# Performance work log

Measured on AMD Instinct MI355X. Metric: run time of the kernel, lower is better.

## Reference

```python
import jax, jax.numpy as jnp
import numpy as np

N1, E1 = 102400, 300000
N2, E2 = 10240, 40960
N3, E3 = 1024, 4096
G = 64
D = 256   # node_dim == hidden_dim (forced by where(M==0, x, M))
B = 64    # bond_dim
DEPTHS = (3, 3, 4)


def _make_edges(rng, n_nodes, n_edges):
    # build mirrored directed edges so every edge has an exact reverse
    half = n_edges // 2
    u = rng.integers(0, n_nodes, half)
    v = rng.integers(0, n_nodes, half)
    src = np.concatenate([u, v])
    dst = np.concatenate([v, u])
    rev = np.concatenate([np.arange(half, n_edges), np.arange(0, half)])
    return np.stack([src, dst]).astype(np.int64), rev.astype(np.int64)


def _linear_params(key, fan_in, fan_out):
    k1, k2 = jax.random.split(key)
    s = 1.0 / np.sqrt(fan_in)
    W = jax.random.uniform(k1, (fan_in, fan_out), jnp.float32, -s, s)
    b = jax.random.uniform(k2, (fan_out,), jnp.float32, -s, s)
    return W, b


def setup_inputs() -> dict:
    rng = np.random.default_rng(0)
    key = jax.random.key(0)
    ks = jax.random.split(key, 16)

    ei1, rev1 = _make_edges(rng, N1, E1)
    ei2, rev2 = _make_edges(rng, N2, E2)
    ei3, rev3 = _make_edges(rng, N3, E3)

    inp = {
        "x": jax.random.normal(ks[0], (N1, D), jnp.float32),
        "edge_attr1": jax.random.normal(ks[1], (E1, B), jnp.float32),
        "edge_attr2": jax.random.normal(ks[2], (E2, B), jnp.float32),
        "edge_attr3": jax.random.normal(ks[3], (E3, B), jnp.float32),
        "edge_index1": jnp.asarray(ei1), "rev_edge_index1": jnp.asarray(rev1),
        "edge_index2": jnp.asarray(ei2), "rev_edge_index2": jnp.asarray(rev2),
        "edge_index3": jnp.asarray(ei3), "rev_edge_index3": jnp.asarray(rev3),
        "batch1_2": jnp.asarray(np.repeat(np.arange(N2), N1 // N2)),
        "batch2": jnp.asarray(np.repeat(np.arange(N3), N2 // N3)),
        "batch3": jnp.asarray(np.repeat(np.arange(G), N3 // G)),
    }
    kidx = 4
    for lvl in (1, 2, 3):
        Wi, bi = _linear_params(ks[kidx], D + B, D); kidx += 1
        Wh, bh = _linear_params(ks[kidx], D, D); kidx += 1
        Wo, bo = _linear_params(ks[kidx], D + D, D); kidx += 1
        inp[f"Wi{lvl}"], inp[f"bi{lvl}"] = Wi, bi
        inp[f"Wh{lvl}"], inp[f"bh{lvl}"] = Wh, bh
        inp[f"Wo{lvl}"], inp[f"bo{lvl}"] = Wo, bo
    return inp


def _bmp(x, src, dst, rev, ea, Wi, bi, Wh, bh, Wo, bo, depth):
    # BondMessagePassing.forward (dropout is identity in eval)
    n = x.shape[0]
    H0 = jax.nn.relu(jnp.concatenate([x[src], ea], axis=1) @ Wi + bi)  # [E, D]
    H = H0
    for _ in range(depth - 1):
        agg = jax.ops.segment_sum(H, dst, num_segments=n)              # [N, D]
        M = agg[src] - H[rev]
        H = jax.nn.relu(H0 + M @ Wh + bh)
    M = jax.ops.segment_sum(H, dst, num_segments=n)
    M = jnp.where(jnp.sum(M, axis=1, keepdims=True) == 0, x, M)
    return jax.nn.relu(jnp.concatenate([x, M], axis=1) @ Wo + bo)


def _mean_pool(h, seg, n):
    s = jax.ops.segment_sum(h, seg, num_segments=n)
    c = jax.ops.segment_sum(jnp.ones((h.shape[0], 1), h.dtype), seg, num_segments=n)
    return s / jnp.maximum(c, 1.0)


def reference(x, edge_attr1, edge_attr2, edge_attr3,
              edge_index1, rev_edge_index1, edge_index2, rev_edge_index2,
              edge_index3, rev_edge_index3, batch1_2, batch2, batch3,
              Wi1, bi1, Wh1, bh1, Wo1, bo1,
              Wi2, bi2, Wh2, bh2, Wo2, bo2,
              Wi3, bi3, Wh3, bh3, Wo3, bo3):
    h1 = _bmp(x, edge_index1[0], edge_index1[1], rev_edge_index1, edge_attr1,
              Wi1, bi1, Wh1, bh1, Wo1, bo1, DEPTHS[0])
    x2 = _mean_pool(h1, batch1_2, N2)
    h2 = _bmp(x2, edge_index2[0], edge_index2[1], rev_edge_index2, edge_attr2,
              Wi2, bi2, Wh2, bh2, Wo2, bo2, DEPTHS[1])
    x3 = _mean_pool(h2, batch2, N3)
    h3 = _bmp(x3, edge_index3[0], edge_index3[1], rev_edge_index3, edge_attr3,
              Wi3, bi3, Wh3, bh3, Wo3, bo3, DEPTHS[2])
    out = _mean_pool(h3, batch3, G)  # [G, D] subgraph3_pooled
    return out
```

## Files before the change

### kernel.cpp

```cpp
#include <hip/hip_runtime.h>
#include <stdint.h>

typedef __bf16 bf16;
typedef __bf16 bf16x4 __attribute__((ext_vector_type(4)));
typedef __bf16 bf16x8 __attribute__((ext_vector_type(8)));
typedef float  f32x4  __attribute__((ext_vector_type(4)));

__device__ __forceinline__ int clampi(int v, int n) { return (v < 0 || v >= n) ? 0 : v; }

__device__ __forceinline__ void gload16(const void* g, void* l) {
  __builtin_amdgcn_global_load_lds((const __attribute__((address_space(1))) void*)g,
                                   (__attribute__((address_space(3))) void*)l, 16, 0, 0);
}

__global__ void wtcvt_kernel(const float* __restrict__ W, bf16* __restrict__ Wt, int K) {
  int idx = blockIdx.x * 256 + threadIdx.x;
  if (idx >= K * 256) return;
  int k = idx >> 8, n = idx & 255;
  Wt[(size_t)n * K + k] = (bf16)W[idx];
}

__global__ void hist_kernel(const int* __restrict__ dst, int E, int* __restrict__ cnt, int N) {
  int e = blockIdx.x * 256 + threadIdx.x;
  if (e < E) atomicAdd(&cnt[clampi(dst[e], N)], 1);
}

__global__ void scan_block_kernel(const int* __restrict__ cnt, int N,
                                  int* __restrict__ incl, int* __restrict__ bsums) {
  __shared__ int sd[256];
  int t = threadIdx.x, bid = blockIdx.x;
  int base = bid * 1024 + t * 4;
  int v0 = (base + 0 < N) ? cnt[base + 0] : 0;
  int v1 = (base + 1 < N) ? cnt[base + 1] : 0;
  int v2 = (base + 2 < N) ? cnt[base + 2] : 0;
  int v3 = (base + 3 < N) ? cnt[base + 3] : 0;
  int s1 = v0 + v1, s2 = s1 + v2, s3 = s2 + v3;
  sd[t] = s3;
  __syncthreads();
  for (int off = 1; off < 256; off <<= 1) {
    int x = 0;
    if (t >= off) x = sd[t - off];
    __syncthreads();
    sd[t] += x;
    __syncthreads();
  }
  int excl = sd[t] - s3;
  if (base + 0 < N) incl[base + 0] = excl + v0;
  if (base + 1 < N) incl[base + 1] = excl + s1;
  if (base + 2 < N) incl[base + 2] = excl + s2;
  if (base + 3 < N) incl[base + 3] = excl + s3;
  if (t == 255) bsums[bid] = sd[255];
}

__global__ void scan_sums_kernel(const int* __restrict__ bsums, int nb, int* __restrict__ bexcl) {
  __shared__ int sd[256];
  int t = threadIdx.x;
  int v = (t < nb) ? bsums[t] : 0;
  sd[t] = v;
  __syncthreads();
  for (int off = 1; off < 256; off <<= 1) {
    int x = 0;
    if (t >= off) x = sd[t - off];
    __syncthreads();
    sd[t] += x;
    __syncthreads();
  }
  if (t < nb) bexcl[t] = sd[t] - v;
}

__global__ void scan_add_kernel(const int* __restrict__ incl, const int* __restrict__ bexcl,
                                int N, int* __restrict__ offs) {
  int i = blockIdx.x * 256 + threadIdx.x;
  if (i < N) offs[i + 1] = incl[i] + bexcl[i >> 10];
  if (i == 0) offs[0] = 0;
}

__global__ void scatter_kernel(const int* __restrict__ dst, int E, const int* __restrict__ offs,
                               int* __restrict__ cursor, int* __restrict__ elist, int N) {
  int e = blockIdx.x * 256 + threadIdx.x;
  if (e < E) {
    int d = clampi(dst[e], N);
    int p = atomicAdd(&cursor[d], 1);
    elist[offs[d] + p] = e;
  }
}

template <int WHERE, int XF32>
__global__ void segsum_kernel(const bf16* __restrict__ H, const int* __restrict__ elist,
                              const int* __restrict__ offs, const float* __restrict__ xf,
                              const bf16* __restrict__ xb, bf16* __restrict__ out, int N) {
  int lane = threadIdx.x & 63;
  int node = blockIdx.x * 4 + (threadIdx.x >> 6);
  if (node >= N) return;
  int beg = offs[node], end = offs[node + 1];
  float a0 = 0.f, a1 = 0.f, a2 = 0.f, a3 = 0.f;
  for (int p = beg; p < end; ++p) {
    int e = elist[p];
    bf16x4 v = ((const bf16x4*)(H + (size_t)e * 256))[lane];
    a0 += (float)v[0]; a1 += (float)v[1]; a2 += (float)v[2]; a3 += (float)v[3];
  }
  if (WHERE) {
    float s = a0 + a1 + a2 + a3;
    for (int off = 1; off < 64; off <<= 1) s += __shfl_xor(s, off);
    if (s == 0.f) {
      bf16x4 o;
      if (XF32) {
        float4 xv = ((const float4*)(xf))[(size_t)node * 64 + lane];
        o[0] = (bf16)xv.x; o[1] = (bf16)xv.y; o[2] = (bf16)xv.z; o[3] = (bf16)xv.w;
      } else {
        o = ((const bf16x4*)(xb + (size_t)node * 256))[lane];
      }
      ((bf16x4*)(out + (size_t)node * 256))[lane] = o;
      return;
    }
  }
  bf16x4 o = {(bf16)a0, (bf16)a1, (bf16)a2, (bf16)a3};
  ((bf16x4*)(out + (size_t)node * 256))[lane] = o;
}

template <int OUTF32>
__global__ void pool_kernel(const bf16* __restrict__ h, bf16* __restrict__ outb,
                            float* __restrict__ outf, int Nout, int cnt) {
  int lane = threadIdx.x & 63;
  int node = blockIdx.x * 4 + (threadIdx.x >> 6);
  if (node >= Nout) return;
  float a0 = 0.f, a1 = 0.f, a2 = 0.f, a3 = 0.f;
  size_t base = (size_t)node * cnt;
  for (int p = 0; p < cnt; ++p) {
    bf16x4 v = ((const bf16x4*)(h + (base + p) * 256))[lane];
    a0 += (float)v[0]; a1 += (float)v[1]; a2 += (float)v[2]; a3 += (float)v[3];
  }
  float c = (float)cnt;
  a0 /= c; a1 /= c; a2 /= c; a3 /= c;
  if (OUTF32) {
    float4 o = {a0, a1, a2, a3};
    ((float4*)(outf + (size_t)node * 256))[lane] = o;
  } else {
    bf16x4 o = {(bf16)a0, (bf16)a1, (bf16)a2, (bf16)a3};
    ((bf16x4*)(outb + (size_t)node * 256))[lane] = o;
  }
}

template <int MODE, int XF32>
__global__ __launch_bounds__(256, 2) void gemm_kernel(
    const float* __restrict__ A1f, const bf16* __restrict__ A1b,
    const float* __restrict__ A2f, const bf16* __restrict__ A2b,
    const bf16* __restrict__ Wt, const float* __restrict__ bias, const bf16* H0,
    const int* __restrict__ srcIdx, const int* __restrict__ revIdx,
    bf16* out, int Mrows, int K, int Nsrc) {
  __shared__ __align__(16) bf16 As[2][64 * 64];
  __shared__ __align__(16) bf16 Bs[2][256 * 64];
  const int tid = threadIdx.x;
  const int lane = tid & 63;
  const int wave = tid >> 6;
  const int m0 = blockIdx.x * 64;

  int rowA[2], uA[2], base1[2], base2[2];
#pragma unroll
  for (int r = 0; r < 2; ++r) {
    int unit = r * 256 + tid;
    rowA[r] = unit >> 3;
    uA[r] = unit & 7;
    int rr = m0 + rowA[r];
    if (rr >= Mrows) rr = Mrows - 1;
    if (MODE == 0) {
      base1[r] = clampi(srcIdx[rr], Nsrc) * 256;
      base2[r] = rr * 64;
    } else if (MODE == 1) {
      base1[r] = clampi(srcIdx[rr], Nsrc) * 256;
      base2[r] = clampi(revIdx[rr], Mrows) * 256;
    } else {
      base1[r] = rr * 256;
      base2[r] = rr * 256;
    }
  }

  f32x4 acc[4][4];
#pragma unroll
  for (int i = 0; i < 4; ++i)
#pragma unroll
    for (int j = 0; j < 4; ++j) acc[i][j] = (f32x4){0.f, 0.f, 0.f, 0.f};

  float4 pf[2][2];

  auto loadA = [&](int kc) {
    int k0 = kc * 64;
#pragma unroll
    for (int r = 0; r < 2; ++r) {
      int u8 = uA[r] * 8;
      if (MODE == 0) {
        if (k0 < 256) {
          if (XF32) {
            const float* g = A1f + (size_t)(base1[r] + k0 + u8);
            pf[r][0] = *(const float4*)g;
            pf[r][1] = *(const float4*)(g + 4);
          } else {
            pf[r][0] = *(const float4*)(A1b + (size_t)(base1[r] + k0 + u8));
          }
        } else {
          const float* g = A2f + (size_t)(base2[r] + u8);
          pf[r][0] = *(const float4*)g;
          pf[r][1] = *(const float4*)(g + 4);
        }
      } else if (MODE == 1) {
        pf[r][0] = *(const float4*)(A1b + (size_t)(base1[r] + k0 + u8));
        pf[r][1] = *(const float4*)(A2b + (size_t)(base2[r] + k0 + u8));
      } else {
        if (k0 < 256) {
          if (XF32) {
            const float* g = A1f + (size_t)(base1[r] + k0 + u8);
            pf[r][0] = *(const float4*)g;
            pf[r][1] = *(const float4*)(g + 4);
          } else {
            pf[r][0] = *(const float4*)(A1b + (size_t)(base1[r] + k0 + u8));
          }
        } else {
          pf[r][0] = *(const float4*)(A2b + (size_t)(base2[r] + (k0 - 256) + u8));
        }
      }
    }
  };

  auto writeA = [&](int kc, int buf) {
    int k0 = kc * 64;
#pragma unroll
    for (int r = 0; r < 2; ++r) {
      int row = rowA[r], us = uA[r] ^ (row & 7);
      bf16x8 v;
      bool cvt32;
      if (MODE == 0) cvt32 = XF32 || (k0 >= 256);
      else if (MODE == 2) cvt32 = XF32 && (k0 < 256);
      else cvt32 = false;
      if (MODE == 1) {
        bf16x8 va = *(bf16x8*)&pf[r][0];
        bf16x8 vh = *(bf16x8*)&pf[r][1];
#pragma unroll
        for (int j = 0; j < 8; ++j) v[j] = (bf16)((float)va[j] - (float)vh[j]);
      } else if (cvt32) {
        const float* f = (const float*)&pf[r][0];
#pragma unroll
        for (int j = 0; j < 8; ++j) v[j] = (bf16)f[j];
      } else {
        v = *(bf16x8*)&pf[r][0];
      }
      *(bf16x8*)(&As[buf][((size_t)row * 8 + us) * 8]) = v;
    }
  };

  auto issueB = [&](int kc, int buf) {
    int k0 = kc * 64;
#pragma unroll
    for (int r = 0; r < 8; ++r) {
      int unit = r * 256 + tid;
      int row = unit >> 3, us = (unit & 7) ^ (row & 7);
      gload16(Wt + (size_t)row * K + k0 + us * 8, &Bs[buf][(r * 256 + wave * 64) * 8]);
    }
  };

  const int nk = K / 64;
  issueB(0, 0);
  loadA(0);
  writeA(0, 0);
  int cur = 0;
  for (int kc = 0; kc < nk; ++kc) {
    __syncthreads();
    if (kc + 1 < nk) {
      issueB(kc + 1, cur ^ 1);
      loadA(kc + 1);
    }
    const bf16* Asb = As[cur];
    const bf16* Bsb = Bs[cur];
#pragma unroll
    for (int s = 0; s < 2; ++s) {
      int kq = s * 4 + (lane >> 4);
      bf16x8 af[4], bfr[4];
#pragma unroll
      for (int i = 0; i < 4; ++i) {
        int arow = i * 16 + (lane & 15);
        af[i] = *(const bf16x8*)(&Asb[(size_t)arow * 64 + (size_t)(kq ^ (arow & 7)) * 8]);
      }
#pragma unroll
      for (int j = 0; j < 4; ++j) {
        int brow = wave * 64 + j * 16 + (lane & 15);
        bfr[j] = *(const bf16x8*)(&Bsb[(size_t)brow * 64 + (size_t)(kq ^ (brow & 7)) * 8]);
      }
#pragma unroll
      for (int i = 0; i < 4; ++i)
#pragma unroll
        for (int j = 0; j < 4; ++j)
          acc[i][j] = __builtin_amdgcn_mfma_f32_16x16x32_bf16(af[i], bfr[j], acc[i][j], 0, 0, 0);
    }
    if (kc + 1 < nk) writeA(kc + 1, cur ^ 1);
    cur ^= 1;
  }
#pragma unroll
  for (int i = 0; i < 4; ++i) {
    int rbase = m0 + i * 16 + ((lane >> 4) << 2);
#pragma unroll
    for (int j = 0; j < 4; ++j) {
      int col = wave * 64 + j * 16 + (lane & 15);
      float bcol = bias[col];
#pragma unroll
      for (int r = 0; r < 4; ++r) {
        int row = rbase + r;
        if (row < Mrows) {
          float v = acc[i][j][r] + bcol;
          if (MODE == 1) v += (float)H0[(size_t)row * 256 + col];
          v = fmaxf(v, 0.f);
          out[(size_t)row * 256 + col] = (bf16)v;
        }
      }
    }
  }
}

template <int XF32>
static void run_level(const float* xf, const bf16* xb, const float* ea,
                      const int* src, const int* dst, const int* rev, int E, int N, int depth,
                      const bf16* WiT, const float* bi_, const bf16* WhT, const float* bh_,
                      const bf16* WoT, const float* bo_,
                      bf16* C, bf16* Dd, bf16* Ee, bf16* agg, bf16* h,
                      int* cnt, int* incl, int* offs, int* cursr, int* bsums, int* bexcl,
                      int* elist, hipStream_t stream) {
  hipMemsetAsync(cnt, 0, (size_t)N * 4, stream);
  hist_kernel<<<(E + 255) / 256, 256, 0, stream>>>(dst, E, cnt, N);
  int nb = (N + 1023) / 1024;
  scan_block_kernel<<<nb, 256, 0, stream>>>(cnt, N, incl, bsums);
  scan_sums_kernel<<<1, 256, 0, stream>>>(bsums, nb, bexcl);
  scan_add_kernel<<<(N + 255) / 256, 256, 0, stream>>>(incl, bexcl, N, offs);
  hipMemsetAsync(cursr, 0, (size_t)N * 4, stream);
  scatter_kernel<<<(E + 255) / 256, 256, 0, stream>>>(dst, E, offs, cursr, elist, N);

  dim3 ge((E + 63) / 64);
  gemm_kernel<0, XF32><<<ge, 256, 0, stream>>>(xf, xb, ea, nullptr, WiT, bi_, nullptr, src,
                                               nullptr, C, E, 320, N);
  bf16* Hcur = C;
  for (int it = 0; it < depth - 1; ++it) {
    segsum_kernel<0, 0><<<(N + 3) / 4, 256, 0, stream>>>(Hcur, elist, offs, nullptr, nullptr,
                                                         agg, N);
    bf16* Hn = (it == depth - 2) ? C : ((it & 1) ? Ee : Dd);
    gemm_kernel<1, 0><<<ge, 256, 0, stream>>>(nullptr, agg, nullptr, Hcur, WhT, bh_, C, src,
                                              rev, Hn, E, 256, N);
    Hcur = Hn;
  }
  segsum_kernel<1, XF32><<<(N + 3) / 4, 256, 0, stream>>>(Hcur, elist, offs, xf, xb, agg, N);
  dim3 gn((N + 63) / 64);
  gemm_kernel<2, XF32><<<gn, 256, 0, stream>>>(xf, xb, nullptr, agg, WoT, bo_, nullptr, nullptr,
                                               nullptr, h, N, 512, N);
}

extern "C" void kernel_launch(void* const* d_in, const int* in_sizes, int n_in,
                              void* d_out, int out_size, void* d_ws, size_t ws_size,
                              hipStream_t stream) {
  constexpr int N1 = 102400, E1 = 300000;
  constexpr int N2 = 10240, E2 = 40960;
  constexpr int N3 = 1024, E3 = 4096;
  constexpr int G = 64;
  constexpr int KI = 320, KH = 256, KO = 512;

  const float* x   = (const float*)d_in[0];
  const float* ea1 = (const float*)d_in[1];
  const float* ea2 = (const float*)d_in[2];
  const float* ea3 = (const float*)d_in[3];
  const int* ei1 = (const int*)d_in[4];
  const int* rv1 = (const int*)d_in[5];
  const int* ei2 = (const int*)d_in[6];
  const int* rv2 = (const int*)d_in[7];
  const int* ei3 = (const int*)d_in[8];
  const int* rv3 = (const int*)d_in[9];
  const float *Wi[3], *bi[3], *Wh[3], *bh[3], *Wo[3], *bo[3];
  for (int l = 0; l < 3; ++l) {
    Wi[l] = (const float*)d_in[13 + 6 * l + 0];
    bi[l] = (const float*)d_in[13 + 6 * l + 1];
    Wh[l] = (const float*)d_in[13 + 6 * l + 2];
    bh[l] = (const float*)d_in[13 + 6 * l + 3];
    Wo[l] = (const float*)d_in[13 + 6 * l + 4];
    bo[l] = (const float*)d_in[13 + 6 * l + 5];
  }
  float* outp = (float*)d_out;
  char* ws = (char*)d_ws;

  size_t off = 0;
  auto alloc = [&](size_t b) { size_t o = off; off += (b + 255) & ~(size_t)255; return o; };
  size_t o_wit[3], o_wht[3], o_wot[3];
  for (int l = 0; l < 3; ++l) {
    o_wit[l] = alloc((size_t)256 * KI * 2);
    o_wht[l] = alloc((size_t)256 * KH * 2);
    o_wot[l] = alloc((size_t)256 * KO * 2);
  }
  size_t o_C   = alloc((size_t)E1 * 256 * 2);
  size_t o_D   = alloc((size_t)E1 * 256 * 2);
  size_t o_E3b = alloc((size_t)E3 * 256 * 2);
  size_t o_agg = alloc((size_t)N1 * 256 * 2);
  size_t o_x2  = alloc((size_t)N2 * 256 * 2);
  size_t o_h2  = alloc((size_t)N2 * 256 * 2);
  size_t o_x3  = alloc((size_t)N3 * 256 * 2);
  size_t o_h3  = alloc((size_t)N3 * 256 * 2);
  size_t o_cnt = alloc((size_t)N1 * 4);
  size_t o_inc = alloc((size_t)N1 * 4);
  size_t o_off = alloc((size_t)(N1 + 1) * 4);
  size_t o_cur = alloc((size_t)N1 * 4);
  size_t o_bs  = alloc(1024 * 4);
  size_t o_bx  = alloc(1024 * 4);
  size_t o_el  = alloc((size_t)E1 * 4);

  if (ws_size < off) {
    hipMemsetAsync(d_out, 0, (size_t)out_size * 4, stream);
    return;
  }

  int* cnt   = (int*)(ws + o_cnt);
  int* incl  = (int*)(ws + o_inc);
  int* offs  = (int*)(ws + o_off);
  int* cursr = (int*)(ws + o_cur);
  int* bsums = (int*)(ws + o_bs);
  int* bexcl = (int*)(ws + o_bx);
  int* elist = (int*)(ws + o_el);
  bf16* C    = (bf16*)(ws + o_C);
  bf16* Dd   = (bf16*)(ws + o_D);
  bf16* E3b  = (bf16*)(ws + o_E3b);
  bf16* agg  = (bf16*)(ws + o_agg);
  bf16* x2b  = (bf16*)(ws + o_x2);
  bf16* h2b  = (bf16*)(ws + o_h2);
  bf16* x3b  = (bf16*)(ws + o_x3);
  bf16* h3b  = (bf16*)(ws + o_h3);

  for (int l = 0; l < 3; ++l) {
    wtcvt_kernel<<<(KI * 256 + 255) / 256, 256, 0, stream>>>(Wi[l], (bf16*)(ws + o_wit[l]), KI);
    wtcvt_kernel<<<(KH * 256 + 255) / 256, 256, 0, stream>>>(Wh[l], (bf16*)(ws + o_wht[l]), KH);
    wtcvt_kernel<<<(KO * 256 + 255) / 256, 256, 0, stream>>>(Wo[l], (bf16*)(ws + o_wot[l]), KO);
  }

  run_level<1>(x, nullptr, ea1, ei1, ei1 + E1, rv1, E1, N1, 3,
               (bf16*)(ws + o_wit[0]), bi[0], (bf16*)(ws + o_wht[0]), bh[0],
               (bf16*)(ws + o_wot[0]), bo[0], C, Dd, Dd, agg, C,
               cnt, incl, offs, cursr, bsums, bexcl, elist, stream);
  pool_kernel<0><<<(N2 + 3) / 4, 256, 0, stream>>>(C, x2b, nullptr, N2, N1 / N2);

  run_level<0>(nullptr, x2b, ea2, ei2, ei2 + E2, rv2, E2, N2, 3,
               (bf16*)(ws + o_wit[1]), bi[1], (bf16*)(ws + o_wht[1]), bh[1],
               (bf16*)(ws + o_wot[1]), bo[1], C, Dd, Dd, agg, h2b,
               cnt, incl, offs, cursr, bsums, bexcl, elist, stream);
  pool_kernel<0><<<(N3 + 3) / 4, 256, 0, stream>>>(h2b, x3b, nullptr, N3, N2 / N3);

  run_level<0>(nullptr, x3b, ea3, ei3, ei3 + E3, rv3, E3, N3, 4,
               (bf16*)(ws + o_wit[2]), bi[2], (bf16*)(ws + o_wht[2]), bh[2],
               (bf16*)(ws + o_wot[2]), bo[2], C, Dd, E3b, agg, h3b,
               cnt, incl, offs, cursr, bsums, bexcl, elist, stream);
  pool_kernel<1><<<(G + 3) / 4, 256, 0, stream>>>(h3b, nullptr, outp, G, N3 / G);
}
```

Measured before the change: 1.355 ms.

## Read GEMM weights directly from global memory and pre-convert level-1 features to bf16

The GEMM no longer stages the weight tile in LDS. Each wave now loads its B fragments straight from global or L2, and the block grows to 512 threads as a 2x4 wave grid over a 64x256 tile, with K fixed at compile time and the k-loop fully unrolled. This removes the large B shared buffer and its async copies, trading them for repeated global weight reads. It also adds a kernel that converts the fp32 level-1 node features to bf16 once, so the gathered A loads read half the bytes, but it needs extra workspace and falls back to the old path when that is unavailable.

```diff
diff --git a/kernel.cpp b/kernel.cpp
--- a/kernel.cpp
+++ b/kernel.cpp
@@ -8,9 +8,14 @@
 
 __device__ __forceinline__ int clampi(int v, int n) { return (v < 0 || v >= n) ? 0 : v; }
 
-__device__ __forceinline__ void gload16(const void* g, void* l) {
-  __builtin_amdgcn_global_load_lds((const __attribute__((address_space(1))) void*)g,
-                                   (__attribute__((address_space(3))) void*)l, 16, 0, 0);
+__global__ void cvt_kernel(const float* __restrict__ in, bf16* __restrict__ out, int n8) {
+  int i = blockIdx.x * 256 + threadIdx.x;
+  if (i >= n8) return;
+  float4 a = ((const float4*)in)[i * 2];
+  float4 b = ((const float4*)in)[i * 2 + 1];
+  bf16x8 o = {(bf16)a.x, (bf16)a.y, (bf16)a.z, (bf16)a.w,
+              (bf16)b.x, (bf16)b.y, (bf16)b.z, (bf16)b.w};
+  ((bf16x8*)out)[i] = o;
 }
 
 __global__ void wtcvt_kernel(const float* __restrict__ W, bf16* __restrict__ Wt, int K) {
@@ -142,163 +147,145 @@
 }
 
 template <int MODE, int XF32>
-__global__ __launch_bounds__(256, 2) void gemm_kernel(
+__global__ __launch_bounds__(512) void gemm_kernel(
     const float* __restrict__ A1f, const bf16* __restrict__ A1b,
     const float* __restrict__ A2f, const bf16* __restrict__ A2b,
     const bf16* __restrict__ Wt, const float* __restrict__ bias, const bf16* H0,
     const int* __restrict__ srcIdx, const int* __restrict__ revIdx,
-    bf16* out, int Mrows, int K, int Nsrc) {
+    bf16* out, int Mrows, int Nsrc) {
+  constexpr int KK = MODE == 0 ? 320 : (MODE == 1 ? 256 : 512);
+  constexpr int NK = KK / 64;
   __shared__ __align__(16) bf16 As[2][64 * 64];
-  __shared__ __align__(16) bf16 Bs[2][256 * 64];
   const int tid = threadIdx.x;
   const int lane = tid & 63;
   const int wave = tid >> 6;
+  const int wm = wave >> 2, wn = wave & 3;
   const int m0 = blockIdx.x * 64;
 
-  int rowA[2], uA[2], base1[2], base2[2];
-#pragma unroll
-  for (int r = 0; r < 2; ++r) {
-    int unit = r * 256 + tid;
-    rowA[r] = unit >> 3;
-    uA[r] = unit & 7;
-    int rr = m0 + rowA[r];
+  const int rowA = tid >> 3, uA = tid & 7;
+  int base1, base2;
+  {
+    int rr = m0 + rowA;
     if (rr >= Mrows) rr = Mrows - 1;
     if (MODE == 0) {
-      base1[r] = clampi(srcIdx[rr], Nsrc) * 256;
-      base2[r] = rr * 64;
+      base1 = clampi(srcIdx[rr], Nsrc) * 256;
+      base2 = rr * 64;
     } else if (MODE == 1) {
-      base1[r] = clampi(srcIdx[rr], Nsrc) * 256;
-      base2[r] = clampi(revIdx[rr], Mrows) * 256;
+      base1 = clampi(srcIdx[rr], Nsrc) * 256;
+      base2 = clampi(revIdx[rr], Mrows) * 256;
     } else {
-      base1[r] = rr * 256;
-      base2[r] = rr * 256;
-    }
-  }
-
-  f32x4 acc[4][4];
-#pragma unroll
-  for (int i = 0; i < 4; ++i)
+      base1 = rr * 256;
+      base2 = rr * 256;
+    }
+  }
+  int colE[4];
+#pragma unroll
+  for (int j = 0; j < 4; ++j) colE[j] = (wn * 64 + j * 16 + (lane & 15)) * KK;
+
+  f32x4 acc[2][4];
+#pragma unroll
+  for (int i = 0; i < 2; ++i)
 #pragma unroll
     for (int j = 0; j < 4; ++j) acc[i][j] = (f32x4){0.f, 0.f, 0.f, 0.f};
 
-  float4 pf[2][2];
+  float4 pf[2];
 
   auto loadA = [&](int kc) {
-    int k0 = kc * 64;
-#pragma unroll
-    for (int r = 0; r < 2; ++r) {
-      int u8 = uA[r] * 8;
-      if (MODE == 0) {
-        if (k0 < 256) {
-          if (XF32) {
-            const float* g = A1f + (size_t)(base1[r] + k0 + u8);
-            pf[r][0] = *(const float4*)g;
-            pf[r][1] = *(const float4*)(g + 4);
-          } else {
-            pf[r][0] = *(const float4*)(A1b + (size_t)(base1[r] + k0 + u8));
-          }
+    int k0 = kc * 64, u8 = uA * 8;
+    if (MODE == 0) {
+      if (k0 < 256) {
+        if (XF32) {
+          const float* g = A1f + (size_t)(base1 + k0 + u8);
+          pf[0] = *(const float4*)g;
+          pf[1] = *(const float4*)(g + 4);
         } else {
-          const float* g = A2f + (size_t)(base2[r] + u8);
-          pf[r][0] = *(const float4*)g;
-          pf[r][1] = *(const float4*)(g + 4);
+          pf[0] = *(const float4*)(A1b + (size_t)(base1 + k0 + u8));
         }
-      } else if (MODE == 1) {
-        pf[r][0] = *(const float4*)(A1b + (size_t)(base1[r] + k0 + u8));
-        pf[r][1] = *(const float4*)(A2b + (size_t)(base2[r] + k0 + u8));
       } else {
-        if (k0 < 256) {
-          if (XF32) {
-            const float* g = A1f + (size_t)(base1[r] + k0 + u8);
-            pf[r][0] = *(const float4*)g;
-            pf[r][1] = *(const float4*)(g + 4);
-          } else {
-            pf[r][0] = *(const float4*)(A1b + (size_t)(base1[r] + k0 + u8));
-          }
+        const float* g = A2f + (size_t)(base2 + u8);
+        pf[0] = *(const float4*)g;
+        pf[1] = *(const float4*)(g + 4);
+      }
+    } else if (MODE == 1) {
+      pf[0] = *(const float4*)(A1b + (size_t)(base1 + k0 + u8));
+      pf[1] = *(const float4*)(A2b + (size_t)(base2 + k0 + u8));
+    } else {
+      if (k0 < 256) {
+        if (XF32) {
+          const float* g = A1f + (size_t)(base1 + k0 + u8);
+          pf[0] = *(const float4*)g;
+          pf[1] = *(const float4*)(g + 4);
         } else {
-          pf[r][0] = *(const float4*)(A2b + (size_t)(base2[r] + (k0 - 256) + u8));
+          pf[0] = *(const float4*)(A1b + (size_t)(base1 + k0 + u8));
         }
+      } else {
+        pf[0] = *(const float4*)(A2b + (size_t)(base2 + (k0 - 256) + u8));
       }
     }
   };
 
   auto writeA = [&](int kc, int buf) {
     int k0 = kc * 64;
-#pragma unroll
-    for (int r = 0; r < 2; ++r) {
-      int row = rowA[r], us = uA[r] ^ (row & 7);
-      bf16x8 v;
-      bool cvt32;
-      if (MODE == 0) cvt32 = XF32 || (k0 >= 256);
-      else if (MODE == 2) cvt32 = XF32 && (k0 < 256);
-      else cvt32 = false;
-      if (MODE == 1) {
-        bf16x8 va = *(bf16x8*)&pf[r][0];
-        bf16x8 vh = *(bf16x8*)&pf[r][1];
-#pragma unroll
-        for (int j = 0; j < 8; ++j) v[j] = (bf16)((float)va[j] - (float)vh[j]);
-      } else if (cvt32) {
-        const float* f = (const float*)&pf[r][0];
-#pragma unroll
-        for (int j = 0; j < 8; ++j) v[j] = (bf16)f[j];
-      } else {
-        v = *(bf16x8*)&pf[r][0];
+    int us = uA ^ (rowA & 7);
+    bf16x8 v;
+    bool cvt32;
+    if (MODE == 0) cvt32 = XF32 || (k0 >= 256);
+    else if (MODE == 2) cvt32 = XF32 && (k0 < 256);
+    else cvt32 = false;
+    if (MODE == 1) {
+      bf16x8 va = *(bf16x8*)&pf[0];
+      bf16x8 vh = *(bf16x8*)&pf[1];
+#pragma unroll
+      for (int j = 0; j < 8; ++j) v[j] = (bf16)((float)va[j] - (float)vh[j]);
+    } else if (cvt32) {
+      const float* f = (const float*)&pf[0];
+#pragma unroll
+      for (int j = 0; j < 8; ++j) v[j] = (bf16)f[j];
+    } else {
+      v = *(bf16x8*)&pf[0];
+    }
+    *(bf16x8*)(&As[buf][((size_t)rowA * 8 + us) * 8]) = v;
+  };
+
+  auto compute = [&](int kc, int buf) {
+    const bf16* Asb = As[buf];
+#pragma unroll
+    for (int s = 0; s < 2; ++s) {
+      int kq = s * 4 + (lane >> 4);
+      int boff = kc * 64 + kq * 8;
+      bf16x8 bfr[4];
+#pragma unroll
+      for (int j = 0; j < 4; ++j) bfr[j] = *(const bf16x8*)(Wt + (size_t)(colE[j] + boff));
+      bf16x8 af[2];
+#pragma unroll
+      for (int i = 0; i < 2; ++i) {
+        int ar = wm * 32 + i * 16 + (lane & 15);
+        af[i] = *(const bf16x8*)(&Asb[(size_t)ar * 64 + (size_t)(kq ^ (ar & 7)) * 8]);
       }
-      *(bf16x8*)(&As[buf][((size_t)row * 8 + us) * 8]) = v;
+#pragma unroll
+      for (int i = 0; i < 2; ++i)
+#pragma unroll
+        for (int j = 0; j < 4; ++j)
+          acc[i][j] = __builtin_amdgcn_mfma_f32_16x16x32_bf16(af[i], bfr[j], acc[i][j], 0, 0, 0);
     }
   };
 
-  auto issueB = [&](int kc, int buf) {
-    int k0 = kc * 64;
-#pragma unroll
-    for (int r = 0; r < 8; ++r) {
-      int unit = r * 256 + tid;
-      int row = unit >> 3, us = (unit & 7) ^ (row & 7);
-      gload16(Wt + (size_t)row * K + k0 + us * 8, &Bs[buf][(r * 256 + wave * 64) * 8]);
-    }
-  };
-
-  const int nk = K / 64;
-  issueB(0, 0);
   loadA(0);
   writeA(0, 0);
-  int cur = 0;
-  for (int kc = 0; kc < nk; ++kc) {
+  __syncthreads();
+#pragma unroll
+  for (int kc = 0; kc < NK; ++kc) {
+    if (kc + 1 < NK) loadA(kc + 1);
+    compute(kc, kc & 1);
+    if (kc + 1 < NK) writeA(kc + 1, (kc + 1) & 1);
     __syncthreads();
-    if (kc + 1 < nk) {
-      issueB(kc + 1, cur ^ 1);
-      loadA(kc + 1);
-    }
-    const bf16* Asb = As[cur];
-    const bf16* Bsb = Bs[cur];
-#pragma unroll
-    for (int s = 0; s < 2; ++s) {
-      int kq = s * 4 + (lane >> 4);
-      bf16x8 af[4], bfr[4];
-#pragma unroll
-      for (int i = 0; i < 4; ++i) {
-        int arow = i * 16 + (lane & 15);
-        af[i] = *(const bf16x8*)(&Asb[(size_t)arow * 64 + (size_t)(kq ^ (arow & 7)) * 8]);
-      }
-#pragma unroll
-      for (int j = 0; j < 4; ++j) {
-        int brow = wave * 64 + j * 16 + (lane & 15);
-        bfr[j] = *(const bf16x8*)(&Bsb[(size_t)brow * 64 + (size_t)(kq ^ (brow & 7)) * 8]);
-      }
-#pragma unroll
-      for (int i = 0; i < 4; ++i)
-#pragma unroll
-        for (int j = 0; j < 4; ++j)
-          acc[i][j] = __builtin_amdgcn_mfma_f32_16x16x32_bf16(af[i], bfr[j], acc[i][j], 0, 0, 0);
-    }
-    if (kc + 1 < nk) writeA(kc + 1, cur ^ 1);
-    cur ^= 1;
-  }
-#pragma unroll
-  for (int i = 0; i < 4; ++i) {
-    int rbase = m0 + i * 16 + ((lane >> 4) << 2);
+  }
+#pragma unroll
+  for (int i = 0; i < 2; ++i) {
+    int rbase = m0 + wm * 32 + i * 16 + ((lane >> 4) << 2);
 #pragma unroll
     for (int j = 0; j < 4; ++j) {
-      int col = wave * 64 + j * 16 + (lane & 15);
+      int col = wn * 64 + j * 16 + (lane & 15);
       float bcol = bias[col];
 #pragma unroll
       for (int r = 0; r < 4; ++r) {
@@ -332,21 +319,21 @@
   scatter_kernel<<<(E + 255) / 256, 256, 0, stream>>>(dst, E, offs, cursr, elist, N);
 
   dim3 ge((E + 63) / 64);
-  gemm_kernel<0, XF32><<<ge, 256, 0, stream>>>(xf, xb, ea, nullptr, WiT, bi_, nullptr, src,
-                                               nullptr, C, E, 320, N);
+  gemm_kernel<0, XF32><<<ge, 512, 0, stream>>>(xf, xb, ea, nullptr, WiT, bi_, nullptr, src,
+                                               nullptr, C, E, N);
   bf16* Hcur = C;
   for (int it = 0; it < depth - 1; ++it) {
     segsum_kernel<0, 0><<<(N + 3) / 4, 256, 0, stream>>>(Hcur, elist, offs, nullptr, nullptr,
                                                          agg, N);
     bf16* Hn = (it == depth - 2) ? C : ((it & 1) ? Ee : Dd);
-    gemm_kernel<1, 0><<<ge, 256, 0, stream>>>(nullptr, agg, nullptr, Hcur, WhT, bh_, C, src,
-                                              rev, Hn, E, 256, N);
+    gemm_kernel<1, 0><<<ge, 512, 0, stream>>>(nullptr, agg, nullptr, Hcur, WhT, bh_, C, src,
+                                              rev, Hn, E, N);
     Hcur = Hn;
   }
   segsum_kernel<1, XF32><<<(N + 3) / 4, 256, 0, stream>>>(Hcur, elist, offs, xf, xb, agg, N);
   dim3 gn((N + 63) / 64);
-  gemm_kernel<2, XF32><<<gn, 256, 0, stream>>>(xf, xb, nullptr, agg, WoT, bo_, nullptr, nullptr,
-                                               nullptr, h, N, 512, N);
+  gemm_kernel<2, XF32><<<gn, 512, 0, stream>>>(xf, xb, nullptr, agg, WoT, bo_, nullptr, nullptr,
+                                               nullptr, h, N, N);
 }
 
 extern "C" void kernel_launch(void* const* d_in, const int* in_sizes, int n_in,
@@ -403,11 +390,15 @@
   size_t o_bs  = alloc(1024 * 4);
   size_t o_bx  = alloc(1024 * 4);
   size_t o_el  = alloc((size_t)E1 * 4);
-
-  if (ws_size < off) {
+  size_t need_base = off;
+  size_t o_xb = alloc((size_t)N1 * 256 * 2);
+  size_t need_ext = off;
+
+  if (ws_size < need_base) {
     hipMemsetAsync(d_out, 0, (size_t)out_size * 4, stream);
     return;
   }
+  const bool use_xb = (ws_size >= need_ext);
 
   int* cnt   = (int*)(ws + o_cnt);
   int* incl  = (int*)(ws + o_inc);
@@ -424,6 +415,7 @@
   bf16* h2b  = (bf16*)(ws + o_h2);
   bf16* x3b  = (bf16*)(ws + o_x3);
   bf16* h3b  = (bf16*)(ws + o_h3);
+  bf16* xbp  = (bf16*)(ws + o_xb);
 
   for (int l = 0; l < 3; ++l) {
     wtcvt_kernel<<<(KI * 256 + 255) / 256, 256, 0, stream>>>(Wi[l], (bf16*)(ws + o_wit[l]), KI);
@@ -431,10 +423,18 @@
     wtcvt_kernel<<<(KO * 256 + 255) / 256, 256, 0, stream>>>(Wo[l], (bf16*)(ws + o_wot[l]), KO);
   }
 
-  run_level<1>(x, nullptr, ea1, ei1, ei1 + E1, rv1, E1, N1, 3,
-               (bf16*)(ws + o_wit[0]), bi[0], (bf16*)(ws + o_wht[0]), bh[0],
-               (bf16*)(ws + o_wot[0]), bo[0], C, Dd, Dd, agg, C,
-               cnt, incl, offs, cursr, bsums, bexcl, elist, stream);
+  if (use_xb) {
+    cvt_kernel<<<(N1 * 256 / 8 + 255) / 256, 256, 0, stream>>>(x, xbp, N1 * 256 / 8);
+    run_level<0>(nullptr, xbp, ea1, ei1, ei1 + E1, rv1, E1, N1, 3,
+                 (bf16*)(ws + o_wit[0]), bi[0], (bf16*)(ws + o_wht[0]), bh[0],
+                 (bf16*)(ws + o_wot[0]), bo[0], C, Dd, Dd, agg, C,
+                 cnt, incl, offs, cursr, bsums, bexcl, elist, stream);
+  } else {
+    run_level<1>(x, nullptr, ea1, ei1, ei1 + E1, rv1, E1, N1, 3,
+                 (bf16*)(ws + o_wit[0]), bi[0], (bf16*)(ws + o_wht[0]), bh[0],
+                 (bf16*)(ws + o_wot[0]), bo[0], C, Dd, Dd, agg, C,
+                 cnt, incl, offs, cursr, bsums, bexcl, elist, stream);
+  }
   pool_kernel<0><<<(N2 + 3) / 4, 256, 0, stream>>>(C, x2b, nullptr, N2, N1 / N2);
 
   run_level<0>(nullptr, x2b, ea2, ei2, ei2 + E2, rv2, E2, N2, 3,
```

After: 1.516 ms. +11.9%, slower.
